# Kernel tuning notes

Measured on AMD Instinct MI355X. Metric: run time of the kernel, lower is better.

## Reference

```python
import jax, jax.numpy as jnp
import numpy as np

B, S, D = 1, 2048, 2048
H = 32          # num_heads == num_kv_heads (n_rep = 1)
QB = 8          # rosa_num_query_key_bits
VB = 8          # rosa_num_value_bits
TAU = 1.0


def setup_inputs() -> dict:
    key = jax.random.key(0)
    ks = jax.random.split(key, 8)
    s = 0.02
    return {
        "hidden_states": jax.random.normal(ks[0], (B, S, D), dtype=jnp.float32),
        "Wq": jax.random.normal(ks[1], (D, H * QB), dtype=jnp.float32) * s,
        "Wk": jax.random.normal(ks[2], (D, H * QB), dtype=jnp.float32) * s,
        "Wv": jax.random.normal(ks[3], (D, H * VB), dtype=jnp.float32) * s,
        "Wo": jax.random.normal(ks[4], (H * VB, D), dtype=jnp.float32) * s,
        "Wg": jax.random.normal(ks[5], (D, D), dtype=jnp.float32) * s,
        "v_emb0": jnp.full((H * VB,), -1e-05, dtype=jnp.float32),
        "v_emb1": jnp.full((H * VB,), +1e-05, dtype=jnp.float32),
    }


def _rosa_attention(hs, Wq, Wk, Wv, Wo, Wg, v_emb0, v_emb1):
    b, s, _ = hs.shape
    # low-bit projections -> [B, H, S, bits]
    q = (hs @ Wq).reshape(b, s, H, QB).transpose(0, 2, 1, 3)
    k = (hs @ Wk).reshape(b, s, H, QB).transpose(0, 2, 1, 3)
    v = (hs @ Wv).reshape(b, s, H, VB).transpose(0, 2, 1, 3)
    # soft-binarized bit probabilities (training-mode relaxation, temperature tau)
    pq = jax.nn.sigmoid(q / TAU)
    pk = jax.nn.sigmoid(k / TAU)
    pv = jax.nn.sigmoid(v / TAU)
    # expected number of matching bits:
    # sum_d pq*pk + (1-pq)*(1-pk) = 2*<pq,pk> - sum(pq) - sum(pk) + QB
    dot = jnp.einsum('bhqd,bhkd->bhqk', pq, pk)
    scores = 2.0 * dot - pq.sum(-1)[..., :, None] - pk.sum(-1)[..., None, :] + QB
    # causal mask
    causal = jnp.tril(jnp.ones((s, s), dtype=bool))
    scores = jnp.where(causal, scores / TAU, jnp.finfo(scores.dtype).min)
    attn = jax.nn.softmax(scores, axis=-1)
    out = jnp.einsum('bhqk,bhkd->bhqd', attn, pv)           # [B,H,S,VB], in (0,1)
    out = out.transpose(0, 2, 1, 3).reshape(b, s, H * VB)
    # binary value-embedding interpolation
    out = v_emb1 * out + v_emb0 * (1.0 - out)
    out = out @ Wo
    gate = jax.nn.sigmoid(hs @ Wg)
    return out * gate


def reference(hidden_states, Wq, Wk, Wv, Wo, Wg, v_emb0, v_emb1):
    return _rosa_attention(hidden_states, Wq, Wk, Wv, Wo, Wg, v_emb0, v_emb1)
```

## Files before the change

kernel.cpp:

```cpp
#include <hip/hip_runtime.h>

#define S 2048
#define DIM 2048
#define H 32
#define NB 2816

using u16 = unsigned short;
using short8 = __attribute__((ext_vector_type(8))) short;
using f32x4 = __attribute__((ext_vector_type(4))) float;

__device__ __forceinline__ u16 f2bf(float x) {
  union { float f; unsigned u; } v; v.f = x;
  unsigned r = v.u + 0x7fffu + ((v.u >> 16) & 1u);
  return (u16)(r >> 16);
}
__device__ __forceinline__ float sigm(float x) { return 1.f / (1.f + __expf(-x)); }

#define GLOAD_LDS16(g, l)                                                      \
  __builtin_amdgcn_global_load_lds(                                            \
      (const __attribute__((address_space(1))) unsigned*)(g),                  \
      (__attribute__((address_space(3))) unsigned*)(l), 16, 0, 0)

__global__ __launch_bounds__(256)
void trans_all_k(const float* __restrict__ Wq, const float* __restrict__ Wk,
                 const float* __restrict__ Wv, const float* __restrict__ Wg,
                 const float* __restrict__ Wo, const float* __restrict__ hs,
                 u16* __restrict__ Wt, u16* __restrict__ Wot, u16* __restrict__ Abf) {
  int b = blockIdx.x;
  const int t = threadIdx.x;
  if (b >= 1536) {
    int i = ((b - 1536) * 256 + t) * 8;
    float4 a = *(const float4*)(hs + i);
    float4 c = *(const float4*)(hs + i + 4);
    uint4 r;
    r.x = f2bf(a.x) | ((unsigned)f2bf(a.y) << 16);
    r.y = f2bf(a.z) | ((unsigned)f2bf(a.w) << 16);
    r.z = f2bf(c.x) | ((unsigned)f2bf(c.y) << 16);
    r.w = f2bf(c.z) | ((unsigned)f2bf(c.w) << 16);
    *(uint4*)(Abf + i) = r;
    return;
  }
  const float* in; u16* out; int K, N;
  if (b < 384) {
    K = 2048; N = 256;
    in = (b < 128) ? Wq : (b < 256) ? Wk : Wv;
    out = Wt + (size_t)(b >> 7) * 256 * 2048;
    b &= 127;
  } else if (b < 1408) {
    in = Wg; out = Wt + (size_t)768 * 2048; K = 2048; N = 2048; b -= 384;
  } else {
    in = Wo; out = Wot; K = 256; N = 2048; b -= 1408;
  }
  const int nbN = N >> 6;
  const int kb = (b / nbN) << 6, nb = (b % nbN) << 6;
  __shared__ float tile[64][65];
  const int n4 = (t & 15) * 4;
#pragma unroll
  for (int p = 0; p < 4; p++) {
    int k = p * 16 + (t >> 4);
    float4 v = *(const float4*)(in + (size_t)(kb + k) * N + nb + n4);
    tile[k][n4] = v.x; tile[k][n4 + 1] = v.y; tile[k][n4 + 2] = v.z; tile[k][n4 + 3] = v.w;
  }
  __syncthreads();
  const int k8 = (t & 7) * 8;
#pragma unroll
  for (int p = 0; p < 2; p++) {
    int n = p * 32 + (t >> 3);
    uint4 w;
    w.x = f2bf(tile[k8 + 0][n]) | ((unsigned)f2bf(tile[k8 + 1][n]) << 16);
    w.y = f2bf(tile[k8 + 2][n]) | ((unsigned)f2bf(tile[k8 + 3][n]) << 16);
    w.z = f2bf(tile[k8 + 4][n]) | ((unsigned)f2bf(tile[k8 + 5][n]) << 16);
    w.w = f2bf(tile[k8 + 6][n]) | ((unsigned)f2bf(tile[k8 + 7][n]) << 16);
    *(uint4*)(out + (size_t)(nb + n) * K + kb + k8) = w;
  }
}

__global__ __launch_bounds__(256)
void gemm128_k(const u16* __restrict__ A, const u16* __restrict__ Bt,
               float* __restrict__ C, int K, int ldc) {
  __shared__ u16 As[2][128][32];
  __shared__ u16 Bs[2][128][32];
  const int t = threadIdx.x;
  const int bm = blockIdx.y * 128, bn = blockIdx.x * 128;
  const int wave = t >> 6, lane = t & 63;
  const int wm = (wave >> 1) * 64, wn = (wave & 1) * 64;
  const int l16 = lane & 15, quad = lane >> 4;
  const int srow = t >> 2, scol = (t & 3) * 8;
  const u16* Ap = A + (size_t)(bm + srow) * K + scol;
  const u16* Bp = Bt + (size_t)(bn + srow) * K + scol;
  f32x4 acc[4][4];
#pragma unroll
  for (int i = 0; i < 4; i++)
#pragma unroll
    for (int j = 0; j < 4; j++) acc[i][j] = (f32x4){0.f, 0.f, 0.f, 0.f};
  GLOAD_LDS16(Ap, &As[0][srow][scol]);
  GLOAD_LDS16(Ap + (size_t)64 * K, &As[0][srow + 64][scol]);
  GLOAD_LDS16(Bp, &Bs[0][srow][scol]);
  GLOAD_LDS16(Bp + (size_t)64 * K, &Bs[0][srow + 64][scol]);
  for (int kk = 0; kk < K; kk += 32) {
    const int cur = (kk >> 5) & 1, nxt = cur ^ 1;
    __syncthreads();
    if (kk + 32 < K) {
      GLOAD_LDS16(Ap + kk + 32, &As[nxt][srow][scol]);
      GLOAD_LDS16(Ap + (size_t)64 * K + kk + 32, &As[nxt][srow + 64][scol]);
      GLOAD_LDS16(Bp + kk + 32, &Bs[nxt][srow][scol]);
      GLOAD_LDS16(Bp + (size_t)64 * K + kk + 32, &Bs[nxt][srow + 64][scol]);
    }
    short8 af[4], bf[4];
#pragma unroll
    for (int mt = 0; mt < 4; mt++) af[mt] = *(const short8*)&As[cur][wm + mt * 16 + l16][quad * 8];
#pragma unroll
    for (int nt = 0; nt < 4; nt++) bf[nt] = *(const short8*)&Bs[cur][wn + nt * 16 + l16][quad * 8];
#pragma unroll
    for (int mt = 0; mt < 4; mt++)
#pragma unroll
      for (int nt = 0; nt < 4; nt++)
        acc[mt][nt] = __builtin_amdgcn_mfma_f32_16x16x32_bf16(af[mt], bf[nt], acc[mt][nt], 0, 0, 0);
  }
#pragma unroll
  for (int mt = 0; mt < 4; mt++)
#pragma unroll
    for (int nt = 0; nt < 4; nt++)
#pragma unroll
      for (int r = 0; r < 4; r++) {
        int m = bm + wm + mt * 16 + quad * 4 + r;
        int n = bn + wn + nt * 16 + l16;
        float v = acc[mt][nt][r];
        C[(size_t)m * ldc + n] = 1.f / (1.f + __expf(-v));
      }
}

__global__ __launch_bounds__(256)
void gemm64_k(const u16* __restrict__ A, const u16* __restrict__ Bt,
              float* __restrict__ C, const float* __restrict__ gate,
              int K, int ldc) {
  __shared__ u16 As[2][64][32];
  __shared__ u16 Bs[2][64][32];
  const int t = threadIdx.x;
  const int bm = blockIdx.y * 64, bn = blockIdx.x * 64;
  const int wave = t >> 6, lane = t & 63;
  const int wm = (wave >> 1) * 32, wn = (wave & 1) * 32;
  const int l16 = lane & 15, quad = lane >> 4;
  const int srow = t >> 2, scol = (t & 3) * 8;
  const u16* Ap = A + (size_t)(bm + srow) * K + scol;
  const u16* Bp = Bt + (size_t)(bn + srow) * K + scol;
  f32x4 acc[2][2];
#pragma unroll
  for (int i = 0; i < 2; i++)
#pragma unroll
    for (int j = 0; j < 2; j++) acc[i][j] = (f32x4){0.f, 0.f, 0.f, 0.f};
  GLOAD_LDS16(Ap, &As[0][srow][scol]);
  GLOAD_LDS16(Bp, &Bs[0][srow][scol]);
  for (int kk = 0; kk < K; kk += 32) {
    const int cur = (kk >> 5) & 1, nxt = cur ^ 1;
    __syncthreads();
    if (kk + 32 < K) {
      GLOAD_LDS16(Ap + kk + 32, &As[nxt][srow][scol]);
      GLOAD_LDS16(Bp + kk + 32, &Bs[nxt][srow][scol]);
    }
    short8 af[2], bf[2];
#pragma unroll
    for (int mt = 0; mt < 2; mt++) af[mt] = *(const short8*)&As[cur][wm + mt * 16 + l16][quad * 8];
#pragma unroll
    for (int nt = 0; nt < 2; nt++) bf[nt] = *(const short8*)&Bs[cur][wn + nt * 16 + l16][quad * 8];
#pragma unroll
    for (int mt = 0; mt < 2; mt++)
#pragma unroll
      for (int nt = 0; nt < 2; nt++)
        acc[mt][nt] = __builtin_amdgcn_mfma_f32_16x16x32_bf16(af[mt], bf[nt], acc[mt][nt], 0, 0, 0);
  }
#pragma unroll
  for (int mt = 0; mt < 2; mt++)
#pragma unroll
    for (int nt = 0; nt < 2; nt++)
#pragma unroll
      for (int r = 0; r < 4; r++) {
        int m = bm + wm + mt * 16 + quad * 4 + r;
        int n = bn + wn + nt * 16 + l16;
        float v = acc[mt][nt][r] * gate[(size_t)m * NB + n];
        C[(size_t)m * ldc + n] = v;
      }
}

__global__ __launch_bounds__(256)
void attn_mfma_k(const float* __restrict__ P, float* __restrict__ Part) {
  __shared__ u16 Plds[128 * 128];
  __shared__ u16 Vt[16 * 264];
  __shared__ u16 Klds[256 * 8];
  __shared__ u16 Qlds[128 * 8];
  __shared__ float sk2[256];
  const int h = blockIdx.y;
  int tau = blockIdx.x, m = 0;
  while (tau >= (m >> 1) + 1) { tau -= (m >> 1) + 1; m++; }
  const int kc = tau;
  const bool needMask = (kc == (m >> 1));
  const int q0 = m * 128, kb = kc * 256;
  const int t = threadIdx.x, wave = t >> 6, lane = t & 63;
  const int l16 = lane & 15, quad = lane >> 4;
  if (t < 128) {
    const float* rq = P + (size_t)(q0 + t) * NB + h * 8;
    float4 a = *(const float4*)rq, b = *(const float4*)(rq + 4);
    uint4 w;
    w.x = f2bf(a.x) | ((unsigned)f2bf(a.y) << 16);
    w.y = f2bf(a.z) | ((unsigned)f2bf(a.w) << 16);
    w.z = f2bf(b.x) | ((unsigned)f2bf(b.y) << 16);
    w.w = f2bf(b.z) | ((unsigned)f2bf(b.w) << 16);
    *(uint4*)&Qlds[t * 8] = w;
  }
  {
    const float* rk = P + (size_t)(kb + t) * NB + 256 + h * 8;
    float4 k0 = *(const float4*)rk, k1 = *(const float4*)(rk + 4);
    float4 v0 = *(const float4*)(rk + 256), v1 = *(const float4*)(rk + 260);
    sk2[t] = (k0.x + k0.y + k0.z + k0.w + k1.x + k1.y + k1.z + k1.w) * 1.44269504f;
    uint4 w;
    w.x = f2bf(k0.x) | ((unsigned)f2bf(k0.y) << 16);
    w.y = f2bf(k0.z) | ((unsigned)f2bf(k0.w) << 16);
    w.z = f2bf(k1.x) | ((unsigned)f2bf(k1.y) << 16);
    w.w = f2bf(k1.z) | ((unsigned)f2bf(k1.w) << 16);
    *(uint4*)&Klds[t * 8] = w;
    Vt[0 * 264 + t] = f2bf(v0.x); Vt[1 * 264 + t] = f2bf(v0.y);
    Vt[2 * 264 + t] = f2bf(v0.z); Vt[3 * 264 + t] = f2bf(v0.w);
    Vt[4 * 264 + t] = f2bf(v1.x); Vt[5 * 264 + t] = f2bf(v1.y);
    Vt[6 * 264 + t] = f2bf(v1.z); Vt[7 * 264 + t] = f2bf(v1.w);
    Vt[8 * 264 + t] = 0x3F80;
#pragma unroll
    for (int d = 9; d < 16; d++) Vt[d * 264 + t] = 0;
  }
  __syncthreads();
  short8 bq[2];
#pragma unroll
  for (int i = 0; i < 2; i++) {
    short8 z = {0, 0, 0, 0, 0, 0, 0, 0};
    if (quad == 0) z = *(const short8*)&Qlds[((wave * 2 + i) * 16 + l16) * 8];
    bq[i] = z;
  }
  f32x4 O[2];
  O[0] = (f32x4){0.f, 0.f, 0.f, 0.f};
  O[1] = (f32x4){0.f, 0.f, 0.f, 0.f};
  const int nsl = needMask ? (m & 1) + 1 : 2;
  const int swz = (l16 >> 1) & 7;
  for (int sl = 0; sl < nsl; sl++) {
    const int ks = sl * 128;
    const bool dm = needMask && (sl == (m & 1));
    for (int kt = 0; kt < 8; kt++) {
      short8 ak = {0, 0, 0, 0, 0, 0, 0, 0};
      if (quad == 0) ak = *(const short8*)&Klds[(ks + kt * 16 + l16) * 8];
      float4 s2 = *(const float4*)&sk2[ks + kt * 16 + quad * 4];
#pragma unroll
      for (int i = 0; i < 2; i++) {
        f32x4 c = __builtin_amdgcn_mfma_f32_16x16x32_bf16(
            ak, bq[i], (f32x4){0.f, 0.f, 0.f, 0.f}, 0, 0, 0);
        float e0 = exp2f(c[0] * 2.88539008f - s2.x);
        float e1 = exp2f(c[1] * 2.88539008f - s2.y);
        float e2 = exp2f(c[2] * 2.88539008f - s2.z);
        float e3 = exp2f(c[3] * 2.88539008f - s2.w);
        if (dm) {
          int q = q0 + (wave * 2 + i) * 16 + l16;
          int key = kb + ks + kt * 16 + quad * 4;
          e0 = (key + 0 <= q) ? e0 : 0.f;
          e1 = (key + 1 <= q) ? e1 : 0.f;
          e2 = (key + 2 <= q) ? e2 : 0.f;
          e3 = (key + 3 <= q) ? e3 : 0.f;
        }
        uint2 pk2;
        pk2.x = f2bf(e0) | ((unsigned)f2bf(e1) << 16);
        pk2.y = f2bf(e2) | ((unsigned)f2bf(e3) << 16);
        int row = (wave * 2 + i) * 16 + l16;
        int cb = 2 * kt + (quad >> 1);
        int pb = cb ^ swz;
        *(uint2*)&Plds[row * 128 + pb * 8 + (quad & 1) * 4] = pk2;
      }
    }
#pragma unroll
    for (int kc4 = 0; kc4 < 4; kc4++) {
      short8 bv = *(const short8*)&Vt[l16 * 264 + ks + kc4 * 32 + quad * 8];
#pragma unroll
      for (int i = 0; i < 2; i++) {
        int row = (wave * 2 + i) * 16 + l16;
        int pb = (kc4 * 4 + quad) ^ swz;
        short8 ap = *(const short8*)&Plds[row * 128 + pb * 8];
        O[i] = __builtin_amdgcn_mfma_f32_16x16x32_bf16(ap, bv, O[i], 0, 0, 0);
      }
    }
  }
  if (l16 < 9) {
#pragma unroll
    for (int i = 0; i < 2; i++) {
      int qb = q0 + (wave * 2 + i) * 16 + quad * 4;
#pragma unroll
      for (int r = 0; r < 4; r++)
        Part[(((size_t)h * S + qb + r) * 8 + kc) * 12 + l16] = O[i][r];
    }
  }
}

__global__ __launch_bounds__(256)
void attn_merge_k(const float* __restrict__ Part, const float* __restrict__ e0,
                  const float* __restrict__ e1, u16* __restrict__ O2) {
  const int q = blockIdx.x;
  const int t = threadIdx.x;
  const int d = t & 7;
  const int nch = (q >> 8) + 1;
  size_t base = ((size_t)(t >> 3) * S + q) * 8 * 12;
  float ov = 0.f, lv = 0.f;
  for (int kc = 0; kc < nch; kc++) {
    ov += Part[base + (size_t)kc * 12 + d];
    lv += Part[base + (size_t)kc * 12 + 8];
  }
  float outv = ov / lv;
  float r = e0[t] + (e1[t] - e0[t]) * outv;
  O2[(size_t)q * 256 + t] = f2bf(r);
}

extern "C" void kernel_launch(void* const* d_in, const int* in_sizes, int n_in,
                              void* d_out, int out_size, void* d_ws, size_t ws_size,
                              hipStream_t stream) {
  const float* hs = (const float*)d_in[0];
  const float* Wq = (const float*)d_in[1];
  const float* Wk = (const float*)d_in[2];
  const float* Wv = (const float*)d_in[3];
  const float* Wo = (const float*)d_in[4];
  const float* Wg = (const float*)d_in[5];
  const float* e0 = (const float*)d_in[6];
  const float* e1 = (const float*)d_in[7];
  float* out = (float*)d_out;
  char* ws = (char*)d_ws;
  u16*   Abf  = (u16*)(ws + 0);
  u16*   Wt   = (u16*)(ws + 8388608);
  u16*   Wot  = (u16*)(ws + 19922944);
  u16*   O2   = (u16*)(ws + 20971520);
  float* P    = (float*)(ws + 22020096);
  float* Part = (float*)(ws + 45088768);

  trans_all_k<<<dim3(3584), 256, 0, stream>>>(Wq, Wk, Wv, Wg, Wo, hs, Wt, Wot, Abf);
  gemm128_k<<<dim3(NB / 128, S / 128), 256, 0, stream>>>(Abf, Wt, P, 2048, NB);
  attn_mfma_k<<<dim3(72, H), 256, 0, stream>>>(P, Part);
  attn_merge_k<<<dim3(S), 256, 0, stream>>>(Part, e0, e1, O2);
  gemm64_k<<<dim3(DIM / 64, S / 64), 256, 0, stream>>>(O2, Wot, out, P + 768, 256, DIM);
}
```

Baseline: 191.2 us.

## Deepen projection GEMM K-tile to 64 with XOR-swizzled bf16 layout

The fused projection GEMM now stages 64-wide K slices per iteration instead of 32, which halves the number of barriers and gives each wave twice as many MFMAs between syncs. The conversion kernel writes activations and projection weights in an XOR-swizzled column order within each 64-element chunk. That lets the GEMM read LDS fragments without bank conflicts while still using direct global-to-LDS loads. It doubles LDS use per block (64 KB), which may lower occupancy, and ties the data layout to the swizzled producer.

```diff
diff --git a/kernel.cpp b/kernel.cpp
--- a/kernel.cpp
+++ b/kernel.cpp
@@ -37,10 +37,13 @@
     r.y = f2bf(a.z) | ((unsigned)f2bf(a.w) << 16);
     r.z = f2bf(c.x) | ((unsigned)f2bf(c.y) << 16);
     r.w = f2bf(c.z) | ((unsigned)f2bf(c.w) << 16);
-    *(uint4*)(Abf + i) = r;
+    int row = i >> 11, k = i & 2047;
+    int dst = (row << 11) + (k & ~63) + ((((k >> 3) & 7) ^ (row & 7)) << 3);
+    *(uint4*)(Abf + dst) = r;
     return;
   }
   const float* in; u16* out; int K, N;
+  bool isWo = false;
   if (b < 384) {
     K = 2048; N = 256;
     in = (b < 128) ? Wq : (b < 256) ? Wk : Wv;
@@ -49,7 +52,7 @@
   } else if (b < 1408) {
     in = Wg; out = Wt + (size_t)768 * 2048; K = 2048; N = 2048; b -= 384;
   } else {
-    in = Wo; out = Wot; K = 256; N = 2048; b -= 1408;
+    in = Wo; out = Wot; isWo = true; K = 256; N = 2048; b -= 1408;
   }
   const int nbN = N >> 6;
   const int kb = (b / nbN) << 6, nb = (b % nbN) << 6;
@@ -71,51 +74,72 @@
     w.y = f2bf(tile[k8 + 2][n]) | ((unsigned)f2bf(tile[k8 + 3][n]) << 16);
     w.z = f2bf(tile[k8 + 4][n]) | ((unsigned)f2bf(tile[k8 + 5][n]) << 16);
     w.w = f2bf(tile[k8 + 6][n]) | ((unsigned)f2bf(tile[k8 + 7][n]) << 16);
-    *(uint4*)(out + (size_t)(nb + n) * K + kb + k8) = w;
-  }
-}
-
-__global__ __launch_bounds__(256)
-void gemm128_k(const u16* __restrict__ A, const u16* __restrict__ Bt,
-               float* __restrict__ C, int K, int ldc) {
-  __shared__ u16 As[2][128][32];
-  __shared__ u16 Bs[2][128][32];
+    if (isWo) {
+      *(uint4*)(out + (size_t)(nb + n) * K + kb + k8) = w;
+    } else {
+      int nr = nb + n;
+      int col = kb + ((((k8 >> 3) ^ (nr & 7))) << 3);
+      *(uint4*)(out + (size_t)nr * 2048 + col) = w;
+    }
+  }
+}
+
+__global__ __launch_bounds__(256)
+void gemm1_k(const u16* __restrict__ A, const u16* __restrict__ Bt,
+             float* __restrict__ C, int K, int ldc) {
+  __shared__ u16 As[2][128][64];
+  __shared__ u16 Bs[2][128][64];
   const int t = threadIdx.x;
   const int bm = blockIdx.y * 128, bn = blockIdx.x * 128;
   const int wave = t >> 6, lane = t & 63;
   const int wm = (wave >> 1) * 64, wn = (wave & 1) * 64;
   const int l16 = lane & 15, quad = lane >> 4;
-  const int srow = t >> 2, scol = (t & 3) * 8;
+  const int srow = t >> 3, scol = (t & 7) * 8;
   const u16* Ap = A + (size_t)(bm + srow) * K + scol;
   const u16* Bp = Bt + (size_t)(bn + srow) * K + scol;
+#define STAGE1(buf, koff)                                                      \
+  do {                                                                         \
+    GLOAD_LDS16(Ap + (koff), &As[buf][srow][scol]);                            \
+    GLOAD_LDS16(Ap + 32 * (size_t)K + (koff), &As[buf][srow + 32][scol]);      \
+    GLOAD_LDS16(Ap + 64 * (size_t)K + (koff), &As[buf][srow + 64][scol]);      \
+    GLOAD_LDS16(Ap + 96 * (size_t)K + (koff), &As[buf][srow + 96][scol]);      \
+    GLOAD_LDS16(Bp + (koff), &Bs[buf][srow][scol]);                            \
+    GLOAD_LDS16(Bp + 32 * (size_t)K + (koff), &Bs[buf][srow + 32][scol]);      \
+    GLOAD_LDS16(Bp + 64 * (size_t)K + (koff), &Bs[buf][srow + 64][scol]);      \
+    GLOAD_LDS16(Bp + 96 * (size_t)K + (koff), &Bs[buf][srow + 96][scol]);      \
+  } while (0)
   f32x4 acc[4][4];
 #pragma unroll
   for (int i = 0; i < 4; i++)
 #pragma unroll
     for (int j = 0; j < 4; j++) acc[i][j] = (f32x4){0.f, 0.f, 0.f, 0.f};
-  GLOAD_LDS16(Ap, &As[0][srow][scol]);
-  GLOAD_LDS16(Ap + (size_t)64 * K, &As[0][srow + 64][scol]);
-  GLOAD_LDS16(Bp, &Bs[0][srow][scol]);
-  GLOAD_LDS16(Bp + (size_t)64 * K, &Bs[0][srow + 64][scol]);
-  for (int kk = 0; kk < K; kk += 32) {
-    const int cur = (kk >> 5) & 1, nxt = cur ^ 1;
+  STAGE1(0, 0);
+  for (int kk = 0; kk < K; kk += 64) {
+    const int cur = (kk >> 6) & 1, nxt = cur ^ 1;
     __syncthreads();
-    if (kk + 32 < K) {
-      GLOAD_LDS16(Ap + kk + 32, &As[nxt][srow][scol]);
-      GLOAD_LDS16(Ap + (size_t)64 * K + kk + 32, &As[nxt][srow + 64][scol]);
-      GLOAD_LDS16(Bp + kk + 32, &Bs[nxt][srow][scol]);
-      GLOAD_LDS16(Bp + (size_t)64 * K + kk + 32, &Bs[nxt][srow + 64][scol]);
-    }
-    short8 af[4], bf[4];
-#pragma unroll
-    for (int mt = 0; mt < 4; mt++) af[mt] = *(const short8*)&As[cur][wm + mt * 16 + l16][quad * 8];
-#pragma unroll
-    for (int nt = 0; nt < 4; nt++) bf[nt] = *(const short8*)&Bs[cur][wn + nt * 16 + l16][quad * 8];
+    if (kk + 64 < K) STAGE1(nxt, kk + 64);
+    short8 af[4][2], bf[4][2];
+#pragma unroll
+    for (int mt = 0; mt < 4; mt++) {
+      int row = wm + mt * 16 + l16;
+      int rs = (row & 7) << 3;
+      af[mt][0] = *(const short8*)&As[cur][row][(quad << 3) ^ rs];
+      af[mt][1] = *(const short8*)&As[cur][row][((quad + 4) << 3) ^ rs];
+    }
+#pragma unroll
+    for (int nt = 0; nt < 4; nt++) {
+      int row = wn + nt * 16 + l16;
+      int rs = (row & 7) << 3;
+      bf[nt][0] = *(const short8*)&Bs[cur][row][(quad << 3) ^ rs];
+      bf[nt][1] = *(const short8*)&Bs[cur][row][((quad + 4) << 3) ^ rs];
+    }
 #pragma unroll
     for (int mt = 0; mt < 4; mt++)
 #pragma unroll
-      for (int nt = 0; nt < 4; nt++)
-        acc[mt][nt] = __builtin_amdgcn_mfma_f32_16x16x32_bf16(af[mt], bf[nt], acc[mt][nt], 0, 0, 0);
+      for (int nt = 0; nt < 4; nt++) {
+        acc[mt][nt] = __builtin_amdgcn_mfma_f32_16x16x32_bf16(af[mt][0], bf[nt][0], acc[mt][nt], 0, 0, 0);
+        acc[mt][nt] = __builtin_amdgcn_mfma_f32_16x16x32_bf16(af[mt][1], bf[nt][1], acc[mt][nt], 0, 0, 0);
+      }
   }
 #pragma unroll
   for (int mt = 0; mt < 4; mt++)
@@ -128,6 +152,7 @@
         float v = acc[mt][nt][r];
         C[(size_t)m * ldc + n] = 1.f / (1.f + __expf(-v));
       }
+#undef STAGE1
 }
 
 __global__ __launch_bounds__(256)
@@ -333,7 +358,7 @@
   float* Part = (float*)(ws + 45088768);
 
   trans_all_k<<<dim3(3584), 256, 0, stream>>>(Wq, Wk, Wv, Wg, Wo, hs, Wt, Wot, Abf);
-  gemm128_k<<<dim3(NB / 128, S / 128), 256, 0, stream>>>(Abf, Wt, P, 2048, NB);
+  gemm1_k<<<dim3(NB / 128, S / 128), 256, 0, stream>>>(Abf, Wt, P, 2048, NB);
   attn_mfma_k<<<dim3(72, H), 256, 0, stream>>>(P, Part);
   attn_merge_k<<<dim3(S), 256, 0, stream>>>(Part, e0, e1, O2);
   gemm64_k<<<dim3(DIM / 64, S / 64), 256, 0, stream>>>(O2, Wot, out, P + 768, 256, DIM);
```

Result: faster. 184.0 us (-3.8%).
